# Optimization experiments

Hardware: AMD Instinct MI355X
Metric: run time of the kernel (lower is better)

The kernel has to match this reference:

```python
import jax, jax.numpy as jnp
import numpy as np

FG_THR = 0.7
BG_THR = 0.3
NUM_PER_IMAGE = 256
NUM_POS_MAX = int(NUM_PER_IMAGE * 0.5)  # positive_ratio = 0.5
BBOX_W = (1.0, 1.0, 1.0, 1.0)
BETA = 1.0 / 9.0


def _permute(t, C):
    # N x (A*C) x H x W -> N x (H*W*A) x C, matching RPNLoss.permute
    N, _, H, W = t.shape
    t = t.reshape(N, -1, C, H, W)
    t = jnp.transpose(t, (0, 3, 4, 1, 2))
    return t.reshape(N, -1, C)


def _iou(a, b):
    # a: [N,4], b: [M,4] -> [N,M] (with +1 box convention, as in source)
    x_tl = jnp.maximum(a[:, None, 0], b[None, :, 0])
    y_tl = jnp.maximum(a[:, None, 1], b[None, :, 1])
    x_rb = jnp.minimum(a[:, None, 2], b[None, :, 2])
    y_rb = jnp.minimum(a[:, None, 3], b[None, :, 3])
    inter = jnp.clip(x_rb - x_tl + 1.0, 0.0) * jnp.clip(y_rb - y_tl + 1.0, 0.0)
    area1 = (a[:, 2] - a[:, 0] + 1.0) * (a[:, 3] - a[:, 1] + 1.0)
    area2 = (b[:, 2] - b[:, 0] + 1.0) * (b[:, 3] - b[:, 1] + 1.0)
    return inter / (area1[:, None] + area2[None, :] - inter)


def _encode(anchors, targets):
    ws = anchors[:, 2] - anchors[:, 0] + 1.0
    hs = anchors[:, 3] - anchors[:, 1] + 1.0
    x_ctr = anchors[:, 0] + 0.5 * ws
    y_ctr = anchors[:, 1] + 0.5 * hs
    t_ws = targets[:, 2] - targets[:, 0] + 1.0
    t_hs = targets[:, 3] - targets[:, 1] + 1.0
    t_x = targets[:, 0] + 0.5 * t_ws
    t_y = targets[:, 1] + 0.5 * t_hs
    wx, wy, ww, wh = BBOX_W
    tx = wx * (t_x - x_ctr) / ws
    ty = wy * (t_y - y_ctr) / hs
    tw = ww * jnp.log(t_ws / ws)
    th = wh * jnp.log(t_hs / hs)
    return jnp.stack([tx, ty, tw, th], axis=1)


def _bce_logits(l, t):
    return jnp.maximum(l, 0.0) - l * t + jnp.log1p(jnp.exp(-jnp.abs(l)))


def _per_image(anchor, logit, breg, size, target, key):
    N = anchor.shape[0]
    ious = _iou(anchor, target)  # [N, M]
    vals = ious.max(axis=1)
    ori = jnp.argmax(ious, axis=1).astype(jnp.int32)
    inds = jnp.where(vals < BG_THR, -1, ori)
    inds = jnp.where((vals >= BG_THR) & (vals < FG_THR), -2, inds)
    # low-quality matches: anchors achieving the per-target max IoU keep their argmax
    col_max = ious.max(axis=0)
    restore = (ious == col_max[None, :]).any(axis=1)
    inds = jnp.where(restore, ori, inds)
    # filter_anchors: keep anchors fully inside the image (size = (h, w))
    inside = (anchor[:, 0] >= 0) & (anchor[:, 1] >= 0) & \
             (anchor[:, 2] <= size[1] - 1.0) & (anchor[:, 3] <= size[0] - 1.0)
    inds = jnp.where(inside, inds, -2)

    pos = inds >= 0
    neg = inds == -1
    # random sampling via random priorities + fixed-size top_k with validity masks
    r = jax.random.uniform(key, (N,))
    pos_vals, pos_idx = jax.lax.top_k(jnp.where(pos, r, -1.0), NUM_POS_MAX)
    valid_pos = pos_vals >= 0.0
    num_pos = valid_pos.sum()
    neg_vals, neg_idx = jax.lax.top_k(jnp.where(neg, r, -1.0), NUM_PER_IMAGE)
    valid_neg = (neg_vals >= 0.0) & (jnp.arange(NUM_PER_IMAGE) < (NUM_PER_IMAGE - num_pos))

    # classification loss terms (BCE with logits); pos target 1, neg target 0
    vp = valid_pos.astype(logit.dtype)
    vn = valid_neg.astype(logit.dtype)
    cls_sum = jnp.sum(_bce_logits(logit[pos_idx], 1.0) * vp) + \
              jnp.sum(_bce_logits(logit[neg_idx], 0.0) * vn)
    count = num_pos + valid_neg.sum()

    m = jnp.clip(inds[pos_idx], 0, None)
    offsets = _encode(anchor[pos_idx], target[m])
    diff = jnp.abs(breg[pos_idx] - offsets)
    sl1 = jnp.where(diff < BETA, 0.5 * diff * diff / BETA, diff - 0.5 * BETA)
    reg_sum = jnp.sum(sl1 * vp[:, None])
    return cls_sum, count, reg_sum


def reference(anchors, logits, bbox_regs, sizes, targets):
    B = anchors.shape[0]
    log = _permute(logits, 1)[..., 0]      # [B, H*W*A]
    breg = _permute(bbox_regs, 4)          # [B, H*W*A, 4]
    keys = jax.random.split(jax.random.key(42), B)
    cls_s, cnt, reg_s = jax.vmap(_per_image)(anchors, log, breg, sizes, targets, keys)
    total = jnp.sum(cnt).astype(anchors.dtype)
    cls_loss = jnp.sum(cls_s) / total
    reg_loss = jnp.sum(reg_s) / total
    return jnp.stack([cls_loss, reg_loss])


def setup_inputs() -> dict:
    key = jax.random.key(0)
    ks = jax.random.split(key, 10)
    B, A, H, W, M = 4, 3, 168, 256, 32
    N = H * W * A
    IMG_H, IMG_W = 800.0, 1333.0
    x1 = jax.random.uniform(ks[0], (B, N)) * 1200.0
    y1 = jax.random.uniform(ks[1], (B, N)) * 700.0
    aw = jax.random.uniform(ks[2], (B, N)) * 300.0 + 16.0
    ah = jax.random.uniform(ks[3], (B, N)) * 300.0 + 16.0
    anchors = jnp.stack([x1, y1, x1 + aw, y1 + ah], axis=-1)  # some out of image -> filtered
    tx1 = jax.random.uniform(ks[4], (B, M)) * 1000.0
    ty1 = jax.random.uniform(ks[5], (B, M)) * 500.0
    tw = jax.random.uniform(ks[6], (B, M)) * 250.0 + 30.0
    th = jax.random.uniform(ks[7], (B, M)) * 200.0 + 30.0
    targets = jnp.stack([tx1, ty1, jnp.minimum(tx1 + tw, IMG_W - 1.0),
                         jnp.minimum(ty1 + th, IMG_H - 1.0)], axis=-1)
    logits = jax.random.normal(ks[8], (B, A, H, W), dtype=jnp.float32)
    bbox_regs = jax.random.normal(ks[9], (B, 4 * A, H, W), dtype=jnp.float32) * 0.1
    sizes = jnp.tile(jnp.array([IMG_H, IMG_W], dtype=jnp.float32), (B, 1))
    return {"anchors": anchors, "logits": logits, "bbox_regs": bbox_regs,
            "sizes": sizes, "targets": targets}
```

## Files before the change

### kernel.cpp

```cpp
#include <hip/hip_runtime.h>
#include <stdint.h>

#define Bn 4
#define An 3
#define Hn 168
#define Wn 256
#define Mn 32
#define HWn (Hn*Wn)
#define Nn (HWn*An)
#define POS_CAP 8192
#define NPERIM 256
#define NPOSMAX 128
#define FG_THR 0.7f
#define BG_THR 0.3f
#define BETA (1.0f/9.0f)

#define NBLK 504
#define NWAVES (NBLK*4)
#define TSEG_CAP 64
#define NSEG_CAP 64
#define XSEG_CAP 256
#define BIN_HOT 960
#define NHOT 64
#define HB_CAP 256
#define CM_STRIDE 16

#define OFF_POSCNT 0
#define OFF_COUNT  8
#define OFF_CLS    9
#define OFF_REG    10
#define OFF_DONEA  11
#define OFF_BINCNT 16
#define OFF_BINBCE 4112
#define OFF_CM     8208
#define ZERO_WORDS 10256
#define OFF_WPCM   10256
#define OFF_TSEGC  268304
#define OFF_NSEGC  276368
#define OFF_XSEGC  284432
#define OFF_PLIST  286448
#define OFF_HBUCK  351984
#define OFF_TSEG   483056
#define OFF_NSEG   2547440
#define OFF_XSEG   3579632

__device__ __forceinline__ uint32_t rotl32(uint32_t v, int n) { return (v << n) | (v >> (32 - n)); }

__device__ __forceinline__ void tf2x32(uint32_t k0, uint32_t k1, uint32_t x0, uint32_t x1,
                                       uint32_t& o0, uint32_t& o1) {
    uint32_t k2 = k0 ^ k1 ^ 0x1BD11BDAu;
    x0 += k0; x1 += k1;
    x0 += x1; x1 = rotl32(x1, 13); x1 ^= x0;
    x0 += x1; x1 = rotl32(x1, 15); x1 ^= x0;
    x0 += x1; x1 = rotl32(x1, 26); x1 ^= x0;
    x0 += x1; x1 = rotl32(x1, 6);  x1 ^= x0;
    x0 += k1; x1 += k2 + 1u;
    x0 += x1; x1 = rotl32(x1, 17); x1 ^= x0;
    x0 += x1; x1 = rotl32(x1, 29); x1 ^= x0;
    x0 += x1; x1 = rotl32(x1, 16); x1 ^= x0;
    x0 += x1; x1 = rotl32(x1, 24); x1 ^= x0;
    x0 += k2; x1 += k0 + 2u;
    x0 += x1; x1 = rotl32(x1, 13); x1 ^= x0;
    x0 += x1; x1 = rotl32(x1, 15); x1 ^= x0;
    x0 += x1; x1 = rotl32(x1, 26); x1 ^= x0;
    x0 += x1; x1 = rotl32(x1, 6);  x1 ^= x0;
    x0 += k0; x1 += k1 + 3u;
    x0 += x1; x1 = rotl32(x1, 17); x1 ^= x0;
    x0 += x1; x1 = rotl32(x1, 29); x1 ^= x0;
    x0 += x1; x1 = rotl32(x1, 16); x1 ^= x0;
    x0 += x1; x1 = rotl32(x1, 24); x1 ^= x0;
    x0 += k1; x1 += k2 + 4u;
    x0 += x1; x1 = rotl32(x1, 13); x1 ^= x0;
    x0 += x1; x1 = rotl32(x1, 15); x1 ^= x0;
    x0 += x1; x1 = rotl32(x1, 26); x1 ^= x0;
    x0 += x1; x1 = rotl32(x1, 6);  x1 ^= x0;
    x0 += k2; x1 += k0 + 5u;
    o0 = x0; o1 = x1;
}

__device__ __forceinline__ uint32_t rng_m23(uint32_t k0, uint32_t k1, uint32_t i) {
    uint32_t o0, o1;
    tf2x32(k0, k1, 0u, i, o0, o1);
    return (o0 ^ o1) >> 9;
}

__device__ __forceinline__ float iou_one(float a0, float a1, float a2, float a3,
                                         float t0, float t1, float t2, float t3) {
    float xtl = fmaxf(a0, t0), ytl = fmaxf(a1, t1);
    float xrb = fminf(a2, t2), yrb = fminf(a3, t3);
    float iw = fmaxf(xrb - xtl + 1.0f, 0.0f);
    float ih = fmaxf(yrb - ytl + 1.0f, 0.0f);
    float inter = iw * ih;
    float area1 = (a2 - a0 + 1.0f) * (a3 - a1 + 1.0f);
    float area2 = (t2 - t0 + 1.0f) * (t3 - t1 + 1.0f);
    return inter * __builtin_amdgcn_rcpf(area1 + area2 - inter);
}

__device__ __forceinline__ float bce0(float l) {
    return fmaxf(l, 0.0f) + log1pf(expf(-fabsf(l)));
}

__device__ __forceinline__ bool sel_less(uint2 a, uint2 b) {
    return (a.x > b.x) || (a.x == b.x && a.y < b.y);
}

__device__ void bitonic_sort_shared(uint2* buf, int n) {
    for (int k = 2; k <= n; k <<= 1) {
        for (int j = k >> 1; j > 0; j >>= 1) {
            for (int t = (int)threadIdx.x; t < n; t += (int)blockDim.x) {
                int ixj = t ^ j;
                if (ixj > t) {
                    uint2 x = buf[t], y = buf[ixj];
                    bool up = ((t & k) == 0);
                    bool sw = up ? sel_less(y, x) : sel_less(x, y);
                    if (sw) { buf[t] = y; buf[ixj] = x; }
                }
            }
            __syncthreads();
        }
    }
}

__global__ void __launch_bounds__(256) k0_init(uint32_t* __restrict__ ws) {
    int i = blockIdx.x * 256 + (int)threadIdx.x;
    if (i < ZERO_WORDS) ws[i] = 0u;
}

__global__ void __launch_bounds__(256) k1_iou(const float* __restrict__ anchors,
                                              const float* __restrict__ targets,
                                              const float* __restrict__ sizes,
                                              const float* __restrict__ logits,
                                              uint32_t* __restrict__ ws) {
    const int b = blockIdx.y, j = blockIdx.x, tid = threadIdx.x;
    const int wid = tid >> 6, lane = tid & 63;
    __shared__ float part[4][Mn];

    uint32_t key0, key1;
    tf2x32(0u, 42u, 0u, (uint32_t)b, key0, key1);

    const int i = j * 256 + tid;
    float4 av = ((const float4*)anchors)[b * Nn + i];

    float rowmax = -1.0f; int ori = 0; uint32_t tie = 0u;
    float mycm = 0.0f;
    #pragma unroll 4
    for (int t = 0; t < Mn; ++t) {
        float4 tv = ((const float4*)targets)[b * Mn + t];
        float io = iou_one(av.x, av.y, av.z, av.w, tv.x, tv.y, tv.z, tv.w);
        if (io > rowmax) { rowmax = io; ori = t; }
        float m0 = io;
        #pragma unroll
        for (int o = 32; o > 0; o >>= 1) m0 = fmaxf(m0, __shfl_xor(m0, o, 64));
        if (lane == t) mycm = m0;
        tie |= (io == m0) ? (1u << t) : 0u;
    }

    const int wimg = j * 4 + wid;
    if (lane < Mn) {
        ws[OFF_WPCM + ((size_t)b * NWAVES + wimg) * 32 + lane] = __float_as_uint(mycm);
        part[wid][lane] = mycm;
    }
    __syncthreads();
    if (tid < Mn) {
        float v = fmaxf(fmaxf(part[0][tid], part[1][tid]),
                        fmaxf(part[2][tid], part[3][tid]));
        atomicMax(&ws[OFF_CM + (b * 32 + tid) * CM_STRIDE], __float_as_uint(v));
    }

    const float sh = sizes[b * 2 + 0], sw = sizes[b * 2 + 1];
    unsigned long long lt_mask = (lane == 63) ? 0x7FFFFFFFFFFFFFFFull
                                              : ((1ull << lane) - 1ull);
    bool inside = (av.x >= 0.0f) && (av.y >= 0.0f) &&
                  (av.z <= sw - 1.0f) && (av.w <= sh - 1.0f);
    bool fg = rowmax >= FG_THR;
    bool bg = rowmax < BG_THR;
    bool posn   = inside && fg;
    bool defern = inside && !fg && (tie != 0u);
    bool negn   = inside && bg && (tie == 0u);
    uint32_t m = rng_m23(key0, key1, (uint32_t)i);

    const int a_ = i % An, hw_ = i / An;
    float lneg = 0.0f;
    if (negn) lneg = logits[(b * An + a_) * HWn + hw_];

    unsigned long long pmask = __ballot(posn);
    if (pmask) {
        int leader = __ffsll((long long)pmask) - 1;
        uint32_t bb = 0;
        if (lane == leader) bb = atomicAdd(&ws[OFF_POSCNT + b], (uint32_t)__popcll(pmask));
        bb = __shfl(bb, leader, 64);
        if (posn) {
            uint32_t p = bb + (uint32_t)__popcll(pmask & lt_mask);
            if (p < POS_CAP)
                ((uint2*)(ws + OFF_PLIST))[(size_t)b * POS_CAP + p] =
                    make_uint2(m, (uint32_t)i | ((uint32_t)ori << 17));
        }
    }
    unsigned long long dmask = __ballot(defern);
    if (defern) {
        uint32_t slot = (uint32_t)__popcll(dmask & lt_mask);
        ((uint4*)(ws + OFF_TSEG))[((size_t)b * NWAVES + wimg) * TSEG_CAP + slot] =
            make_uint4(tie, m,
                       (uint32_t)i | ((uint32_t)ori << 17) | (bg ? (1u << 22) : 0u), 0u);
    }
    unsigned long long nmask = __ballot(negn);
    if (negn) {
        uint32_t slot = (uint32_t)__popcll(nmask & lt_mask);
        ((uint2*)(ws + OFF_NSEG))[((size_t)b * NWAVES + wimg) * NSEG_CAP + slot] =
            make_uint2(m, (uint32_t)i);
        int bin = (int)(m >> 13);
        if (bin >= BIN_HOT) {
            uint32_t s2 = atomicAdd(&ws[OFF_BINCNT + (b << 10) + bin], 1u);
            if (s2 < HB_CAP)
                ((uint2*)(ws + OFF_HBUCK))[((size_t)b * NHOT + (bin - BIN_HOT)) * HB_CAP + s2] =
                    make_uint2(m, (uint32_t)i);
        } else {
            atomicAdd(&ws[OFF_BINCNT + (b << 10) + bin], 1u);
        }
        atomicAdd((float*)&ws[OFF_BINBCE + (b << 10) + bin], bce0(lneg));
    }
    if (lane == 0) {
        ws[OFF_TSEGC + b * NWAVES + wimg] = (uint32_t)__popcll(dmask);
        ws[OFF_NSEGC + b * NWAVES + wimg] = (uint32_t)__popcll(nmask);
    }
}

__global__ void __launch_bounds__(256) k2_resolve(const float* __restrict__ logits,
                                                  uint32_t* __restrict__ ws) {
    const int b = blockIdx.y, j = blockIdx.x, tid = threadIdx.x;
    const int lane = tid & 63;
    __shared__ uint32_t cmb[Mn];
    __shared__ uint32_t eqs[4];
    __shared__ uint32_t cnts[4];
    __shared__ uint32_t sx_cnt;

    if (tid < 4) { eqs[tid] = 0u; cnts[tid] = ws[OFF_TSEGC + b * NWAVES + j * 4 + tid]; }
    if (tid == 0) sx_cnt = 0u;
    if (tid < Mn) cmb[tid] = ws[OFF_CM + (b * 32 + tid) * CM_STRIDE];
    __syncthreads();
    const int total = (int)(cnts[0] + cnts[1] + cnts[2] + cnts[3]);
    if (total > 0) {
        if (tid < 128) {
            int lw = tid >> 5, t2 = tid & 31;
            uint32_t wv = ws[OFF_WPCM + ((size_t)b * NWAVES + j * 4 + lw) * 32 + t2];
            if (wv == cmb[t2]) atomicOr(&eqs[lw], 1u << t2);
        }
        __syncthreads();

        const uint32_t c0 = cnts[0], c1 = cnts[1], c2 = cnts[2], c3 = cnts[3];
        unsigned long long lt_mask = (lane == 63) ? 0x7FFFFFFFFFFFFFFFull
                                                  : ((1ull << lane) - 1ull);
        for (int f = tid; f < total; f += 256) {
            int lw, o;
            if ((uint32_t)f < c0)                { lw = 0; o = f; }
            else if ((uint32_t)f < c0 + c1)      { lw = 1; o = f - (int)c0; }
            else if ((uint32_t)f < c0 + c1 + c2) { lw = 2; o = f - (int)(c0 + c1); }
            else                                 { lw = 3; o = f - (int)(c0 + c1 + c2); }
            uint4 e = ((const uint4*)(ws + OFF_TSEG))
                          [((size_t)b * NWAVES + j * 4 + lw) * TSEG_CAP + o];
            int i = (int)(e.z & 0x1FFFFu);
            bool restored = (e.x & eqs[lw]) != 0u;

            unsigned long long rmask = __ballot(restored);
            if (rmask) {
                int leader = __ffsll((long long)rmask) - 1;
                uint32_t bb = 0;
                if (lane == leader) bb = atomicAdd(&ws[OFF_POSCNT + b], (uint32_t)__popcll(rmask));
                bb = __shfl(bb, leader, 64);
                if (restored) {
                    uint32_t p = bb + (uint32_t)__popcll(rmask & lt_mask);
                    if (p < POS_CAP)
                        ((uint2*)(ws + OFF_PLIST))[(size_t)b * POS_CAP + p] =
                            make_uint2(e.y, e.z & 0x3FFFFFu);
                }
            }
            if (!restored && (e.z & (1u << 22))) {
                uint32_t m = e.y;
                int bin = (int)(m >> 13);
                if (bin >= BIN_HOT) {
                    uint32_t s2 = atomicAdd(&ws[OFF_BINCNT + (b << 10) + bin], 1u);
                    if (s2 < HB_CAP)
                        ((uint2*)(ws + OFF_HBUCK))
                            [((size_t)b * NHOT + (bin - BIN_HOT)) * HB_CAP + s2] =
                                make_uint2(m, (uint32_t)i);
                } else {
                    atomicAdd(&ws[OFF_BINCNT + (b << 10) + bin], 1u);
                }
                int a = i % An, hw = i / An;
                float l = logits[(b * An + a) * HWn + hw];
                atomicAdd((float*)&ws[OFF_BINBCE + (b << 10) + bin], bce0(l));
                uint32_t xs = atomicAdd(&sx_cnt, 1u);
                if (xs < XSEG_CAP)
                    ((uint2*)(ws + OFF_XSEG))[((size_t)b * NBLK + j) * XSEG_CAP + xs] =
                        make_uint2(m, (uint32_t)i);
            }
        }
    }
    __syncthreads();
    if (tid == 0) ws[OFF_XSEGC + b * NBLK + j] = sx_cnt;
}

__global__ void __launch_bounds__(1024) k3_final(const float* __restrict__ anchors,
                                                 const float* __restrict__ targets,
                                                 const float* __restrict__ logits,
                                                 const float* __restrict__ bregs,
                                                 uint32_t* __restrict__ ws,
                                                 float* __restrict__ out) {
    const int b = blockIdx.x, tid = threadIdx.x;
    __shared__ uint32_t csum[1024];
    __shared__ uint2 buf[2048];
    __shared__ float fred[1024];
    __shared__ int s_bd, s_need;
    __shared__ uint32_t s_fcnt;
    float cls = 0.0f, reg = 0.0f;

    csum[tid] = ws[OFF_BINCNT + (b << 10) + tid];
    __syncthreads();
    for (int off = 1; off < 1024; off <<= 1) {
        uint32_t v = csum[tid];
        uint32_t add = (tid + off < 1024) ? csum[tid + off] : 0u;
        __syncthreads();
        csum[tid] = v + add;
        __syncthreads();
    }
    uint32_t pc = ws[OFF_POSCNT + b];
    int num_pos = (pc < (uint32_t)NPOSMAX) ? (int)pc : NPOSMAX;
    int k_neg = NPERIM - num_pos;
    uint32_t total = csum[0];
    if (tid == 0 && (int)total < k_neg) { s_bd = -1; s_need = 0; }
    {
        uint32_t inclv = csum[tid];
        uint32_t nxt = (tid < 1023) ? csum[tid + 1] : 0u;
        if ((int)total >= k_neg && (int)inclv >= k_neg && (int)nxt < k_neg) {
            s_bd = tid; s_need = k_neg - (int)nxt;
        }
    }
    if (tid == 0) {
        int sel_negs = ((int)total < k_neg) ? (int)total : k_neg;
        atomicAdd(&ws[OFF_COUNT], (uint32_t)(num_pos + sel_negs));
    }
    __syncthreads();
    const int bd = s_bd, need = s_need;
    if ((int)tid > bd)
        cls += __uint_as_float(ws[OFF_BINBCE + (b << 10) + tid]);
    __syncthreads();

    if (need > 0) {
        int cnt;
        if (bd >= BIN_HOT) {
            cnt = (int)ws[OFF_BINCNT + (b << 10) + bd];
            if (cnt > HB_CAP) cnt = HB_CAP;
            const uint2* bkt = (const uint2*)(ws + OFF_HBUCK) +
                               ((size_t)b * NHOT + (bd - BIN_HOT)) * HB_CAP;
            for (int t = tid; t < cnt; t += 1024) buf[t] = bkt[t];
        } else {
            if (tid == 0) s_fcnt = 0u;
            __syncthreads();
            for (int w = tid >> 6; w < NWAVES; w += 16) {
                int cw = (int)ws[OFF_NSEGC + b * NWAVES + w];
                const uint2* ns = (const uint2*)(ws + OFF_NSEG) +
                                  ((size_t)b * NWAVES + w) * NSEG_CAP;
                for (int idx = (tid & 63); idx < cw; idx += 64) {
                    uint2 e = ns[idx];
                    if ((int)(e.x >> 13) == bd) {
                        uint32_t q2 = atomicAdd(&s_fcnt, 1u);
                        if (q2 < 2048u) buf[q2] = e;
                    }
                }
            }
            for (int j2 = tid >> 6; j2 < NBLK; j2 += 16) {
                int cx = (int)ws[OFF_XSEGC + b * NBLK + j2];
                if (cx > XSEG_CAP) cx = XSEG_CAP;
                const uint2* xs = (const uint2*)(ws + OFF_XSEG) +
                                  ((size_t)b * NBLK + j2) * XSEG_CAP;
                for (int idx = (tid & 63); idx < cx; idx += 64) {
                    uint2 e = xs[idx];
                    if ((int)(e.x >> 13) == bd) {
                        uint32_t q2 = atomicAdd(&s_fcnt, 1u);
                        if (q2 < 2048u) buf[q2] = e;
                    }
                }
            }
            __syncthreads();
            cnt = (int)s_fcnt; if (cnt > 2048) cnt = 2048;
        }
        int npad = 1; while (npad < cnt) npad <<= 1;
        for (int t = tid; t < npad; t += 1024) if (t >= cnt) buf[t] = make_uint2(0u, 0xFFFFFFFFu);
        __syncthreads();
        bitonic_sort_shared(buf, npad);
        int sel = (need < cnt) ? need : cnt;
        for (int t = tid; t < sel; t += 1024) {
            int i = (int)buf[t].y;
            int a = i % An, hw = i / An;
            float l = logits[(b * An + a) * HWn + hw];
            cls += bce0(l);
        }
    }
    __syncthreads();

    {
        int pci = (pc < (uint32_t)POS_CAP) ? (int)pc : POS_CAP;
        const uint2* plist = (const uint2*)(ws + OFF_PLIST) + (size_t)b * POS_CAP;
        int psel = (pci < NPOSMAX) ? pci : NPOSMAX;
        bool use_buf = false;
        if (pci > NPOSMAX) {
            int n = (pci < 2048) ? pci : 2048;
            for (int t = tid; t < n; t += 1024) buf[t] = plist[t];
            int npad = 1; while (npad < n) npad <<= 1;
            for (int t = tid; t < npad; t += 1024) if (t >= n) buf[t] = make_uint2(0u, 0xFFFFFFFFu);
            __syncthreads();
            bitonic_sort_shared(buf, npad);
            use_buf = true;
            psel = (NPOSMAX < n) ? NPOSMAX : n;
        }
        for (int t = tid; t < psel; t += 1024) {
            uint32_t packed = use_buf ? buf[t].y : plist[t].y;
            int i = (int)(packed & 0x1FFFFu);
            int orit = (int)((packed >> 17) & 0x1Fu);
            int a = i % An, hw = i / An;
            float l = logits[(b * An + a) * HWn + hw];
            cls += fmaxf(l, 0.0f) - l + log1pf(expf(-fabsf(l)));
            float4 avx = ((const float4*)anchors)[b * Nn + i];
            float4 tv = ((const float4*)targets)[b * Mn + orit];
            float aws = avx.z - avx.x + 1.0f, ahs = avx.w - avx.y + 1.0f;
            float axc = avx.x + 0.5f * aws, ayc = avx.y + 0.5f * ahs;
            float tws = tv.z - tv.x + 1.0f, ths = tv.w - tv.y + 1.0f;
            float txc = tv.x + 0.5f * tws, tyc = tv.y + 0.5f * ths;
            float off0 = (txc - axc) / aws;
            float off1 = (tyc - ayc) / ahs;
            float off2 = logf(tws / aws);
            float off3 = logf(ths / ahs);
            float br0 = bregs[(b * 12 + a * 4 + 0) * HWn + hw];
            float br1 = bregs[(b * 12 + a * 4 + 1) * HWn + hw];
            float br2 = bregs[(b * 12 + a * 4 + 2) * HWn + hw];
            float br3 = bregs[(b * 12 + a * 4 + 3) * HWn + hw];
            float d;
            d = fabsf(br0 - off0); reg += (d < BETA) ? 0.5f * d * d / BETA : d - 0.5f * BETA;
            d = fabsf(br1 - off1); reg += (d < BETA) ? 0.5f * d * d / BETA : d - 0.5f * BETA;
            d = fabsf(br2 - off2); reg += (d < BETA) ? 0.5f * d * d / BETA : d - 0.5f * BETA;
            d = fabsf(br3 - off3); reg += (d < BETA) ? 0.5f * d * d / BETA : d - 0.5f * BETA;
        }
    }

    fred[tid] = cls;
    __syncthreads();
    for (int s = 512; s > 0; s >>= 1) {
        if (tid < s) fred[tid] += fred[tid + s];
        __syncthreads();
    }
    if (tid == 0 && fred[0] != 0.0f) atomicAdd((float*)&ws[OFF_CLS], fred[0]);
    __syncthreads();
    fred[tid] = reg;
    __syncthreads();
    for (int s = 512; s > 0; s >>= 1) {
        if (tid < s) fred[tid] += fred[tid + s];
        __syncthreads();
    }
    if (tid == 0) {
        if (fred[0] != 0.0f) atomicAdd((float*)&ws[OFF_REG], fred[0]);
        __threadfence();
        uint32_t old = atomicAdd(&ws[OFF_DONEA], 1u);
        if (old == Bn - 1) {
            float cls_tot = __uint_as_float(atomicAdd(&ws[OFF_CLS], 0u));
            float reg_tot = __uint_as_float(atomicAdd(&ws[OFF_REG], 0u));
            float cnt = (float)atomicAdd(&ws[OFF_COUNT], 0u);
            out[0] = cls_tot / cnt;
            out[1] = reg_tot / cnt;
        }
    }
}

extern "C" void kernel_launch(void* const* d_in, const int* in_sizes, int n_in,
                              void* d_out, int out_size, void* d_ws, size_t ws_size,
                              hipStream_t stream) {
    const float* anchors = (const float*)d_in[0];
    const float* logits  = (const float*)d_in[1];
    const float* bregs   = (const float*)d_in[2];
    const float* sizes   = (const float*)d_in[3];
    const float* targets = (const float*)d_in[4];
    float* out = (float*)d_out;
    uint32_t* ws = (uint32_t*)d_ws;

    k0_init<<<dim3((ZERO_WORDS + 255) / 256), dim3(256), 0, stream>>>(ws);
    k1_iou<<<dim3(NBLK, Bn), dim3(256), 0, stream>>>(anchors, targets, sizes, logits, ws);
    k2_resolve<<<dim3(NBLK, Bn), dim3(256), 0, stream>>>(logits, ws);
    k3_final<<<dim3(Bn), dim3(1024), 0, stream>>>(anchors, targets, logits, bregs, ws, out);
}
```

Measured before the change: 172.3 us.

## Defer negative-sample BCE to final kernel using hot-bucket lists instead of per-bin atomics

Removes the per-bin float atomicAdd of negative BCE values and the scattered logits gathers from the IoU and resolve kernels. The final kernel now computes the BCE only for the selected negatives, reading them from the hot-bin buckets when the threshold bin is in the hot range and no bucket overflowed. Otherwise it falls back to scanning the per-wave segment lists. This moves gather work onto the 4-block final kernel, which could serialize, in exchange for fewer global atomics and logits reads across the whole grid.

```diff
diff --git a/kernel.cpp b/kernel.cpp
--- a/kernel.cpp
+++ b/kernel.cpp
@@ -31,18 +31,17 @@
 #define OFF_REG    10
 #define OFF_DONEA  11
 #define OFF_BINCNT 16
-#define OFF_BINBCE 4112
-#define OFF_CM     8208
-#define ZERO_WORDS 10256
-#define OFF_WPCM   10256
-#define OFF_TSEGC  268304
-#define OFF_NSEGC  276368
-#define OFF_XSEGC  284432
-#define OFF_PLIST  286448
-#define OFF_HBUCK  351984
-#define OFF_TSEG   483056
-#define OFF_NSEG   2547440
-#define OFF_XSEG   3579632
+#define OFF_CM     4112
+#define ZERO_WORDS 6160
+#define OFF_WPCM   6160
+#define OFF_TSEGC  264208
+#define OFF_NSEGC  272272
+#define OFF_XSEGC  280336
+#define OFF_PLIST  282352
+#define OFF_HBUCK  347888
+#define OFF_TSEG   478960
+#define OFF_NSEG   2543344
+#define OFF_XSEG   3575536
 
 __device__ __forceinline__ uint32_t rotl32(uint32_t v, int n) { return (v << n) | (v >> (32 - n)); }
 
@@ -129,7 +128,6 @@
 __global__ void __launch_bounds__(256) k1_iou(const float* __restrict__ anchors,
                                               const float* __restrict__ targets,
                                               const float* __restrict__ sizes,
-                                              const float* __restrict__ logits,
                                               uint32_t* __restrict__ ws) {
     const int b = blockIdx.y, j = blockIdx.x, tid = threadIdx.x;
     const int wid = tid >> 6, lane = tid & 63;
@@ -178,10 +176,6 @@
     bool defern = inside && !fg && (tie != 0u);
     bool negn   = inside && bg && (tie == 0u);
     uint32_t m = rng_m23(key0, key1, (uint32_t)i);
-
-    const int a_ = i % An, hw_ = i / An;
-    float lneg = 0.0f;
-    if (negn) lneg = logits[(b * An + a_) * HWn + hw_];
 
     unsigned long long pmask = __ballot(posn);
     if (pmask) {
@@ -217,7 +211,6 @@
         } else {
             atomicAdd(&ws[OFF_BINCNT + (b << 10) + bin], 1u);
         }
-        atomicAdd((float*)&ws[OFF_BINBCE + (b << 10) + bin], bce0(lneg));
     }
     if (lane == 0) {
         ws[OFF_TSEGC + b * NWAVES + wimg] = (uint32_t)__popcll(dmask);
@@ -225,8 +218,7 @@
     }
 }
 
-__global__ void __launch_bounds__(256) k2_resolve(const float* __restrict__ logits,
-                                                  uint32_t* __restrict__ ws) {
+__global__ void __launch_bounds__(256) k2_resolve(uint32_t* __restrict__ ws) {
     const int b = blockIdx.y, j = blockIdx.x, tid = threadIdx.x;
     const int lane = tid & 63;
     __shared__ uint32_t cmb[Mn];
@@ -286,9 +278,6 @@
                 } else {
                     atomicAdd(&ws[OFF_BINCNT + (b << 10) + bin], 1u);
                 }
-                int a = i % An, hw = i / An;
-                float l = logits[(b * An + a) * HWn + hw];
-                atomicAdd((float*)&ws[OFF_BINBCE + (b << 10) + bin], bce0(l));
                 uint32_t xs = atomicAdd(&sx_cnt, 1u);
                 if (xs < XSEG_CAP)
                     ((uint2*)(ws + OFF_XSEG))[((size_t)b * NBLK + j) * XSEG_CAP + xs] =
@@ -310,7 +299,8 @@
     __shared__ uint32_t csum[1024];
     __shared__ uint2 buf[2048];
     __shared__ float fred[1024];
-    __shared__ int s_bd, s_need;
+    __shared__ uint32_t hcnt[NHOT];
+    __shared__ int s_bd, s_need, s_fb;
     __shared__ uint32_t s_fcnt;
     float cls = 0.0f, reg = 0.0f;
 
@@ -327,7 +317,11 @@
     int num_pos = (pc < (uint32_t)NPOSMAX) ? (int)pc : NPOSMAX;
     int k_neg = NPERIM - num_pos;
     uint32_t total = csum[0];
-    if (tid == 0 && (int)total < k_neg) { s_bd = -1; s_need = 0; }
+    if (tid == 0) {
+        if ((int)total < k_neg) { s_bd = -1; s_need = 0; }
+        s_fb = 0;
+        s_fcnt = 0u;
+    }
     {
         uint32_t inclv = csum[tid];
         uint32_t nxt = (tid < 1023) ? csum[tid + 1] : 0u;
@@ -339,61 +333,95 @@
         int sel_negs = ((int)total < k_neg) ? (int)total : k_neg;
         atomicAdd(&ws[OFF_COUNT], (uint32_t)(num_pos + sel_negs));
     }
+    if (tid < NHOT) hcnt[tid] = ws[OFF_BINCNT + (b << 10) + BIN_HOT + tid];
     __syncthreads();
     const int bd = s_bd, need = s_need;
-    if ((int)tid > bd)
-        cls += __uint_as_float(ws[OFF_BINBCE + (b << 10) + tid]);
-    __syncthreads();
-
-    if (need > 0) {
-        int cnt;
-        if (bd >= BIN_HOT) {
-            cnt = (int)ws[OFF_BINCNT + (b << 10) + bd];
+
+    if (tid < NHOT) {
+        int bin = BIN_HOT + (int)tid;
+        if (bin >= bd && hcnt[tid] > (uint32_t)HB_CAP) s_fb = 1;
+    }
+    if (tid == 0 && bd < BIN_HOT) s_fb = 1;
+    __syncthreads();
+    const int fb = s_fb;
+
+    if (!fb) {
+        const uint2* hbk = (const uint2*)(ws + OFF_HBUCK) + (size_t)b * NHOT * HB_CAP;
+        for (int idx = tid; idx < NHOT * HB_CAP; idx += 1024) {
+            int hb = idx >> 8;
+            int slot = idx & (HB_CAP - 1);
+            int bin = BIN_HOT + hb;
+            if (bin > bd && slot < (int)hcnt[hb]) {
+                int i = (int)hbk[hb * HB_CAP + slot].y;
+                int a = i % An, hw = i / An;
+                cls += bce0(logits[(b * An + a) * HWn + hw]);
+            }
+        }
+        if (need > 0) {
+            int cnt = (int)hcnt[bd - BIN_HOT];
             if (cnt > HB_CAP) cnt = HB_CAP;
-            const uint2* bkt = (const uint2*)(ws + OFF_HBUCK) +
-                               ((size_t)b * NHOT + (bd - BIN_HOT)) * HB_CAP;
+            const uint2* bkt = hbk + (bd - BIN_HOT) * HB_CAP;
             for (int t = tid; t < cnt; t += 1024) buf[t] = bkt[t];
-        } else {
-            if (tid == 0) s_fcnt = 0u;
+            int npad = 1; while (npad < cnt) npad <<= 1;
+            for (int t = tid; t < npad; t += 1024) if (t >= cnt) buf[t] = make_uint2(0u, 0xFFFFFFFFu);
             __syncthreads();
-            for (int w = tid >> 6; w < NWAVES; w += 16) {
-                int cw = (int)ws[OFF_NSEGC + b * NWAVES + w];
-                const uint2* ns = (const uint2*)(ws + OFF_NSEG) +
-                                  ((size_t)b * NWAVES + w) * NSEG_CAP;
-                for (int idx = (tid & 63); idx < cw; idx += 64) {
-                    uint2 e = ns[idx];
-                    if ((int)(e.x >> 13) == bd) {
-                        uint32_t q2 = atomicAdd(&s_fcnt, 1u);
-                        if (q2 < 2048u) buf[q2] = e;
-                    }
+            bitonic_sort_shared(buf, npad);
+            int sel = (need < cnt) ? need : cnt;
+            for (int t = tid; t < sel; t += 1024) {
+                int i = (int)buf[t].y;
+                int a = i % An, hw = i / An;
+                cls += bce0(logits[(b * An + a) * HWn + hw]);
+            }
+        }
+    } else {
+        for (int w = tid >> 6; w < NWAVES; w += 16) {
+            int cw = (int)ws[OFF_NSEGC + b * NWAVES + w];
+            const uint2* ns = (const uint2*)(ws + OFF_NSEG) +
+                              ((size_t)b * NWAVES + w) * NSEG_CAP;
+            for (int idx = (tid & 63); idx < cw; idx += 64) {
+                uint2 e = ns[idx];
+                int bin = (int)(e.x >> 13);
+                if (bin > bd) {
+                    int i = (int)e.y;
+                    int a = i % An, hw = i / An;
+                    cls += bce0(logits[(b * An + a) * HWn + hw]);
+                } else if (bin == bd) {
+                    uint32_t q2 = atomicAdd(&s_fcnt, 1u);
+                    if (q2 < 2048u) buf[q2] = e;
                 }
             }
-            for (int j2 = tid >> 6; j2 < NBLK; j2 += 16) {
-                int cx = (int)ws[OFF_XSEGC + b * NBLK + j2];
-                if (cx > XSEG_CAP) cx = XSEG_CAP;
-                const uint2* xs = (const uint2*)(ws + OFF_XSEG) +
-                                  ((size_t)b * NBLK + j2) * XSEG_CAP;
-                for (int idx = (tid & 63); idx < cx; idx += 64) {
-                    uint2 e = xs[idx];
-                    if ((int)(e.x >> 13) == bd) {
-                        uint32_t q2 = atomicAdd(&s_fcnt, 1u);
-                        if (q2 < 2048u) buf[q2] = e;
-                    }
+        }
+        for (int j2 = tid >> 6; j2 < NBLK; j2 += 16) {
+            int cx = (int)ws[OFF_XSEGC + b * NBLK + j2];
+            if (cx > XSEG_CAP) cx = XSEG_CAP;
+            const uint2* xs = (const uint2*)(ws + OFF_XSEG) +
+                              ((size_t)b * NBLK + j2) * XSEG_CAP;
+            for (int idx = (tid & 63); idx < cx; idx += 64) {
+                uint2 e = xs[idx];
+                int bin = (int)(e.x >> 13);
+                if (bin > bd) {
+                    int i = (int)e.y;
+                    int a = i % An, hw = i / An;
+                    cls += bce0(logits[(b * An + a) * HWn + hw]);
+                } else if (bin == bd) {
+                    uint32_t q2 = atomicAdd(&s_fcnt, 1u);
+                    if (q2 < 2048u) buf[q2] = e;
                 }
             }
+        }
+        __syncthreads();
+        int cnt = (int)s_fcnt; if (cnt > 2048) cnt = 2048;
+        if (need > 0 && cnt > 0) {
+            int npad = 1; while (npad < cnt) npad <<= 1;
+            for (int t = tid; t < npad; t += 1024) if (t >= cnt) buf[t] = make_uint2(0u, 0xFFFFFFFFu);
             __syncthreads();
-            cnt = (int)s_fcnt; if (cnt > 2048) cnt = 2048;
-        }
-        int npad = 1; while (npad < cnt) npad <<= 1;
-        for (int t = tid; t < npad; t += 1024) if (t >= cnt) buf[t] = make_uint2(0u, 0xFFFFFFFFu);
-        __syncthreads();
-        bitonic_sort_shared(buf, npad);
-        int sel = (need < cnt) ? need : cnt;
-        for (int t = tid; t < sel; t += 1024) {
-            int i = (int)buf[t].y;
-            int a = i % An, hw = i / An;
-            float l = logits[(b * An + a) * HWn + hw];
-            cls += bce0(l);
+            bitonic_sort_shared(buf, npad);
+            int sel = (need < cnt) ? need : cnt;
+            for (int t = tid; t < sel; t += 1024) {
+                int i = (int)buf[t].y;
+                int a = i % An, hw = i / An;
+                cls += bce0(logits[(b * An + a) * HWn + hw]);
+            }
         }
     }
     __syncthreads();
@@ -482,7 +510,7 @@
     uint32_t* ws = (uint32_t*)d_ws;
 
     k0_init<<<dim3((ZERO_WORDS + 255) / 256), dim3(256), 0, stream>>>(ws);
-    k1_iou<<<dim3(NBLK, Bn), dim3(256), 0, stream>>>(anchors, targets, sizes, logits, ws);
-    k2_resolve<<<dim3(NBLK, Bn), dim3(256), 0, stream>>>(logits, ws);
+    k1_iou<<<dim3(NBLK, Bn), dim3(256), 0, stream>>>(anchors, targets, sizes, ws);
+    k2_resolve<<<dim3(NBLK, Bn), dim3(256), 0, stream>>>(ws);
     k3_final<<<dim3(Bn), dim3(1024), 0, stream>>>(anchors, targets, logits, bregs, ws, out);
 }
```

Measured after the change: 154.8 us. 10.2% less time.
